# Kernel tuning notes

Measured on AMD Instinct MI355X. Metric: run time of the kernel, lower is better.

## Reference

```python
import jax, jax.numpy as jnp
import numpy as np
import math

NH = 16
SIGMA = 1.5
KS = 7


def _gaussian_blur_16x16(x):
    # x: (N, 16, 16); torchvision GaussianBlur(7, 1.5) with reflect padding
    hx = jnp.arange(KS, dtype=x.dtype) - (KS - 1) / 2.0
    k1 = jnp.exp(-0.5 * (hx / SIGMA) ** 2)
    k1 = k1 / k1.sum()
    k2 = jnp.outer(k1, k1)[None, None]  # (1,1,7,7)
    pad = KS // 2
    xp = jnp.pad(x, ((0, 0), (pad, pad), (pad, pad)), mode='reflect')[:, None]
    y = jax.lax.conv_general_dilated(xp, k2, (1, 1), 'VALID')
    return y[:, 0]


def _normalize(w):
    mn, mx = w.min(), w.max()
    return (w - mn) / (mx - mn)


def _blurred_map(f, b_perm):
    # f, b_perm: (B, 256, 256)
    B = f.shape[0]
    bi = f * b_perm
    bi = bi.reshape(B * 256, 16, 16)
    bl = _gaussian_blur_16x16(bi)
    bl = jnp.clip(_normalize(bl), 0.0, 1.0)
    bl = bl.reshape(B, 256, 256)
    return bl * f * b_perm


def setup_inputs() -> dict:
    key = jax.random.key(0)
    ks = jax.random.split(key, 16)
    B, T, C = 4, 827, 1024
    inp = {
        'x': jax.random.normal(ks[0], (B, T, C), jnp.float32),
        'h': jax.random.normal(ks[1], (B, NH, 827, 827), jnp.float32) * 0.1,
        'f01': jax.random.uniform(ks[2], (B, 256, 256), jnp.float32),
        'f02': jax.random.uniform(ks[3], (B, 256, 256), jnp.float32),
        'f12': jax.random.uniform(ks[4], (B, 256, 256), jnp.float32),
        'b01': jax.random.uniform(ks[5], (B, 256, 256), jnp.float32),
        'b02': jax.random.uniform(ks[6], (B, 256, 256), jnp.float32),
        'b12': jax.random.uniform(ks[7], (B, 256, 256), jnp.float32),
        'Wq': jax.random.normal(ks[8], (C, C), jnp.float32) * 0.02,
        'bq': jnp.zeros((C,), jnp.float32),
        'Wk': jax.random.normal(ks[9], (C, C), jnp.float32) * 0.02,
        'bk': jnp.zeros((C,), jnp.float32),
        'Wv': jax.random.normal(ks[10], (C, C), jnp.float32) * 0.02,
        'bv': jnp.zeros((C,), jnp.float32),
        'Wp': jax.random.normal(ks[11], (C, C), jnp.float32) * 0.02,
        'bp': jnp.zeros((C,), jnp.float32),
    }
    return inp


def reference(x, h, f01, f02, f12, b01, b02, b12,
              Wq, bq, Wk, bk, Wv, bv, Wp, bp):
    B, T, C = x.shape
    hd = C // NH
    # QKV projections -> (B, NH, T, hd)
    def proj(W, b):
        return (x @ W + b).reshape(B, T, NH, hd).transpose(0, 2, 1, 3)
    q, k, v = proj(Wq, bq), proj(Wk, bk), proj(Wv, bv)

    att = jnp.einsum('bhtd,bhsd->bhts', q, k) * (1.0 / math.sqrt(hd))
    att = h[:, :, :T, :T] + att  # adaptive additive bias

    # bidirectional epipolar multiplicative masks with blur
    b01p = jnp.transpose(b01, (0, 2, 1))
    b02p = jnp.transpose(b02, (0, 2, 1))
    b12p = jnp.transpose(b12, (0, 2, 1))
    blur01 = _blurred_map(f01, b01p)[:, None]  # (B,1,256,256), broadcast over heads
    blur02 = _blurred_map(f02, b02p)[:, None]
    blur12 = _blurred_map(f12, b12p)[:, None]

    n1 = min(T - 285, 256)
    att = att.at[:, :, 285:285 + n1, 0:256].multiply(blur01[:, :, :n1])
    if T > 571:
        n2 = T - 571
        att = att.at[:, :, 571:T, 0:256].multiply(blur02[:, :, :n2])
        att = att.at[:, :, 571:T, 286:542].multiply(blur12[:, :, :n2])

    mask = jnp.tril(jnp.ones((T, T), dtype=bool))
    att = jnp.where(mask, att, -jnp.inf)
    att = jax.nn.softmax(att, axis=-1)

    y = jnp.einsum('bhts,bhsd->bhtd', att, v)
    y = y.transpose(0, 2, 1, 3).reshape(B, T, C)
    return y @ Wp + bp
```

## Files before the change

kernel.cpp:

```cpp
#include <hip/hip_runtime.h>
#include <math.h>

using bfrag8 = __attribute__((ext_vector_type(8))) short;
using facc4  = __attribute__((ext_vector_type(4))) float;

#define MFMA16(a,b,c) __builtin_amdgcn_mfma_f32_16x16x32_bf16((a),(b),(c),0,0,0)

#define T_SEQ 827
#define T_PAD 832
#define NHEAD 16
#define NEG_INF (-__builtin_inff())
#define CM_TOT 1179392

static __device__ __forceinline__ unsigned short f2bf(float f) {
    unsigned int x = __float_as_uint(f);
    unsigned int r = x + 0x7FFFu + ((x >> 16) & 1u);
    return (unsigned short)(r >> 16);
}

static __device__ __forceinline__ void gl16(const unsigned short* g, unsigned short* l) {
    __builtin_amdgcn_global_load_lds(
        (const __attribute__((address_space(1))) unsigned int*)g,
        (__attribute__((address_space(3))) unsigned int*)l,
        16, 0, 0);
}

__global__ __launch_bounds__(256) void k_front(const float* __restrict__ x,
                                               unsigned short* __restrict__ x_bf,
                                               float* __restrict__ cm,
                                               unsigned short* q, unsigned short* k,
                                               unsigned short* vT,
                                               const float* __restrict__ Wq,
                                               const float* __restrict__ Wk,
                                               const float* __restrict__ Wv,
                                               const float* __restrict__ Wp,
                                               unsigned short* __restrict__ Wt_out,
                                               const float* f01, const float* f02, const float* f12,
                                               const float* b01, const float* b02, const float* b12,
                                               float* __restrict__ bl,
                                               float* __restrict__ pmm) {
    __shared__ float tile[32][33];
    __shared__ float img[16][17], tmp[16][17];
    __shared__ float smn[4], smx[4];
    int bid = blockIdx.x, tid = threadIdx.x;

    if (bid < 3308) {
        int i = (bid * 256 + tid) * 4;
        float4 v = *reinterpret_cast<const float4*>(x + i);
        ushort4 o;
        o.x = f2bf(v.x); o.y = f2bf(v.y); o.z = f2bf(v.z); o.w = f2bf(v.w);
        *reinterpret_cast<ushort4*>(x_bf + i) = o;
    } else if (bid < 4460) {
        int base = (bid - 3308) * 1024 + tid * 4;
        if (base + 4 <= CM_TOT) {
            float4 one = {1.f, 1.f, 1.f, 1.f};
            *reinterpret_cast<float4*>(cm + base) = one;
        } else {
#pragma unroll
            for (int j = 0; j < 4; ++j)
                if (base + j < CM_TOT) cm[base + j] = 1.f;
        }
    } else if (bid < 4524) {
        int bh = bid - 4460;
        for (int i = tid; i < 320; i += 256) {
            int t = 827 + i / 64, d = i % 64;
            q[((size_t)bh * T_PAD + t) * 64 + d] = 0;
            k[((size_t)bh * T_PAD + t) * 64 + d] = 0;
        }
        for (int i = tid; i < 4096; i += 256) {
            int d = i >> 6, s = 768 + (i & 63);
            vT[((size_t)bh * 64 + d) * T_PAD + s] = 0;
        }
    } else if (bid < 8620) {
        int i = bid - 4524;
        int z = i >> 10, rem = i & 1023;
        int bx = rem & 31, by = rem >> 5;
        const float* W = (z == 0) ? Wq : (z == 1) ? Wk : (z == 2) ? Wv : Wp;
        unsigned short* Wt = Wt_out + (size_t)z * 1048576;
        int tx = tid & 31, ty0 = tid >> 5;
#pragma unroll
        for (int j = 0; j < 4; ++j) {
            int ty = ty0 + j * 8;
            tile[ty][tx] = W[(size_t)(by * 32 + ty) * 1024 + bx * 32 + tx];
        }
        __syncthreads();
#pragma unroll
        for (int j = 0; j < 4; ++j) {
            int ty = ty0 + j * 8;
            Wt[(size_t)(bx * 32 + ty) * 1024 + by * 32 + tx] = f2bf(tile[tx][ty]);
        }
    } else {
        int i = bid - 8620;
        int m = i >> 10, rem = i & 1023, b = rem >> 8, r = rem & 255;
        const float* f  = (m == 0) ? f01 : (m == 1) ? f02 : f12;
        const float* bm = (m == 0) ? b01 : (m == 1) ? b02 : b12;
        int ii = tid >> 4, j = tid & 15;

        float k1[7]; float ks = 0.f;
#pragma unroll
        for (int d = 0; d < 7; ++d) { float hx = (float)d - 3.f; k1[d] = expf(-0.5f * hx * hx / 2.25f); ks += k1[d]; }
#pragma unroll
        for (int d = 0; d < 7; ++d) k1[d] /= ks;

        size_t idx = (size_t)b * 65536 + (size_t)r * 256 + tid;
        float bi = f[idx] * bm[(size_t)b * 65536 + (size_t)tid * 256 + r];
        img[ii][j] = bi;
        __syncthreads();
        float ha = 0.f;
#pragma unroll
        for (int d = 0; d < 7; ++d) { int p = j - 3 + d; p = p < 0 ? -p : (p > 15 ? 30 - p : p); ha += k1[d] * img[ii][p]; }
        tmp[ii][j] = ha;
        __syncthreads();
        float v = 0.f;
#pragma unroll
        for (int d = 0; d < 7; ++d) { int p = ii - 3 + d; p = p < 0 ? -p : (p > 15 ? 30 - p : p); v += k1[d] * tmp[p][j]; }
        bl[(size_t)m * 262144 + idx] = v;

        float mn = v, mx = v;
#pragma unroll
        for (int off = 32; off; off >>= 1) { mn = fminf(mn, __shfl_xor(mn, off)); mx = fmaxf(mx, __shfl_xor(mx, off)); }
        int wid = tid >> 6, lane = tid & 63;
        if (lane == 0) { smn[wid] = mn; smx[wid] = mx; }
        __syncthreads();
        if (tid == 0) {
            mn = fminf(fminf(smn[0], smn[1]), fminf(smn[2], smn[3]));
            mx = fmaxf(fmaxf(smx[0], smx[1]), fmaxf(smx[2], smx[3]));
            pmm[2 * i]     = mn;
            pmm[2 * i + 1] = mx;
        }
    }
}

__global__ __launch_bounds__(256) void k_gemm_qkv(const unsigned short* __restrict__ A,
                                              const unsigned short* __restrict__ Bt,
                                              const float* __restrict__ b0, const float* __restrict__ b1,
                                              const float* __restrict__ b2,
                                              unsigned short* __restrict__ qo, unsigned short* __restrict__ ko,
                                              unsigned short* __restrict__ vo, int M,
                                              const float* f01, const float* f02, const float* f12,
                                              const float* b01, const float* b02, const float* b12,
                                              const float* __restrict__ bl,
                                              const float* __restrict__ pmm,
                                              float* __restrict__ cm) {
    __shared__ unsigned short As[2][4096];
    __shared__ unsigned short Bs[2][4096];
    int bid = blockIdx.x, tid = threadIdx.x;

    if (bid >= 624) {
        int i = bid - 624;
        int m = i >> 10, rem = i & 1023, b = rem >> 8, r = rem & 255;
        float mn = __builtin_inff(), mx = 0.f;
        for (int kk = tid; kk < 1024; kk += 256) {
            int e = m * 1024 + kk;
            mn = fminf(mn, pmm[2 * e]);
            mx = fmaxf(mx, pmm[2 * e + 1]);
        }
#pragma unroll
        for (int off = 32; off; off >>= 1) { mn = fminf(mn, __shfl_xor(mn, off)); mx = fmaxf(mx, __shfl_xor(mx, off)); }
        float* fs = reinterpret_cast<float*>(&As[0][0]);
        int wid = tid >> 6, lane = tid & 63;
        if (lane == 0) { fs[wid] = mn; fs[4 + wid] = mx; }
        __syncthreads();
        mn = fminf(fminf(fs[0], fs[1]), fminf(fs[2], fs[3]));
        mx = fmaxf(fmaxf(fs[4], fs[5]), fmaxf(fs[6], fs[7]));

        const float* f  = (m == 0) ? f01 : (m == 1) ? f02 : f12;
        const float* bm = (m == 0) ? b01 : (m == 1) ? b02 : b12;
        size_t idx = (size_t)b * 65536 + (size_t)r * 256 + tid;
        float w = (bl[(size_t)m * 262144 + idx] - mn) / (mx - mn);
        w = fminf(fmaxf(w, 0.f), 1.f);
        float val = w * f[idx] * bm[(size_t)b * 65536 + (size_t)tid * 256 + r];
        int row = (m == 0) ? r : r + 286;
        int col = (m == 2) ? tid + 286 : tid;
        cm[((size_t)b * 542 + row) * 544 + col] = val;
        return;
    }

    int swz = (bid & 7) * 78 + (bid >> 3);
    int m0 = (swz % 26) * 128, n0 = (swz / 26) * 128;
    int wid = tid >> 6, lane = tid & 63;
    int g = lane >> 4, l15 = lane & 15;
    int wm = wid >> 1, wn = wid & 1;
    facc4 acc[4][4] = {};

    int ar0 = m0 + (tid >> 2); if (ar0 > M - 1) ar0 = M - 1;
    int ar1 = m0 + 64 + (tid >> 2); if (ar1 > M - 1) ar1 = M - 1;
    const unsigned short* Ap0 = A + (size_t)ar0 * 1024 + (tid & 3) * 8;
    const unsigned short* Ap1 = A + (size_t)ar1 * 1024 + (tid & 3) * 8;
    const unsigned short* Bp0 = Bt + (size_t)(n0 + (tid >> 2)) * 1024 + (tid & 3) * 8;
    const unsigned short* Bp1 = Bp0 + (size_t)64 * 1024;

    auto stage = [&](int koff, int buf) {
        gl16(Ap0 + koff, &As[buf][0] + (wid << 9));
        gl16(Ap1 + koff, &As[buf][0] + (wid << 9) + 2048);
        gl16(Bp0 + koff, &Bs[buf][0] + (wid << 9));
        gl16(Bp1 + koff, &Bs[buf][0] + (wid << 9) + 2048);
    };

    stage(0, 0);
    for (int k0 = 0; k0 < 32; ++k0) {
        int cur = k0 & 1;
        bool morek = (k0 + 1 < 32);
        if (morek) {
            stage((k0 + 1) * 32, cur ^ 1);
            asm volatile("s_waitcnt vmcnt(4)" ::: "memory");
        } else {
            asm volatile("s_waitcnt vmcnt(0)" ::: "memory");
        }
        __builtin_amdgcn_s_barrier();
        __builtin_amdgcn_sched_barrier(0);

        bfrag8 af[4], bf[4];
#pragma unroll
        for (int mi = 0; mi < 4; ++mi)
            af[mi] = *reinterpret_cast<const bfrag8*>(&As[cur][(wm * 64 + mi * 16 + l15) * 32 + g * 8]);
#pragma unroll
        for (int ni = 0; ni < 4; ++ni)
            bf[ni] = *reinterpret_cast<const bfrag8*>(&Bs[cur][(wn * 64 + ni * 16 + l15) * 32 + g * 8]);
        __builtin_amdgcn_s_setprio(1);
#pragma unroll
        for (int mi = 0; mi < 4; ++mi)
#pragma unroll
            for (int ni = 0; ni < 4; ++ni)
                acc[mi][ni] = MFMA16(af[mi], bf[ni], acc[mi][ni]);
        __builtin_amdgcn_s_setprio(0);

        __builtin_amdgcn_sched_barrier(0);
        if (morek) __builtin_amdgcn_s_barrier();
    }

    int which = n0 >> 10;
    const float* bb = (which == 0 ? b0 : (which == 1 ? b1 : b2));
#pragma unroll
    for (int mi = 0; mi < 4; ++mi)
#pragma unroll
        for (int ni = 0; ni < 4; ++ni)
#pragma unroll
            for (int r = 0; r < 4; ++r) {
                int row = m0 + wm * 64 + mi * 16 + g * 4 + r;
                if (row >= M) continue;
                int col = n0 + wn * 64 + ni * 16 + l15;
                float v = acc[mi][ni][r] + bb[col & 1023];
                int b = row / T_SEQ, t = row - b * T_SEQ;
                int cc = col & 1023;
                int hh = cc >> 6, d = cc & 63;
                size_t bh = (size_t)(b * NHEAD + hh);
                if (which == 0) {
                    qo[(bh * T_PAD + t) * 64 + d] = f2bf(v);
                } else if (which == 1) {
                    int du = (((d >> 3) ^ (t & 7)) << 3) | (d & 7);
                    ko[(bh * T_PAD + t) * 64 + du] = f2bf(v);
                } else {
                    int sl = t & 63;
                    int su = (((sl >> 3) ^ (d & 7)) << 3) | (t & 7);
                    vo[(bh * 64 + d) * T_PAD + (t - sl) + su] = f2bf(v);
                }
            }
}

__global__ __launch_bounds__(256) void k_proj64(const unsigned short* __restrict__ A,
                                                const unsigned short* __restrict__ Bt,
                                                const float* __restrict__ bias,
                                                float* __restrict__ out, int M) {
    __shared__ unsigned short As[2048];
    __shared__ unsigned short Bs[2048];
    int bid = blockIdx.x, tid = threadIdx.x;
    int swz = (bid & 7) * 104 + (bid >> 3);
    int m0 = (swz % 52) * 64, n0 = (swz / 52) * 64;
    int wid = tid >> 6, lane = tid & 63;
    int g = lane >> 4, l15 = lane & 15;
    int wm = wid >> 1, wn = wid & 1;
    facc4 acc[2][2] = {};

    int ar = m0 + (tid >> 2); if (ar > M - 1) ar = M - 1;
    const unsigned short* Ap = A + (size_t)ar * 1024 + (tid & 3) * 8;
    const unsigned short* Bp = Bt + (size_t)(n0 + (tid >> 2)) * 1024 + (tid & 3) * 8;
    unsigned short* asw = As + (wid << 9);
    unsigned short* bsw = Bs + (wid << 9);

    for (int k0 = 0; k0 < 1024; k0 += 32) {
        if (k0) __syncthreads();
        gl16(Ap + k0, asw);
        gl16(Bp + k0, bsw);
        __syncthreads();
        bfrag8 af[2], bf[2];
#pragma unroll
        for (int mi = 0; mi < 2; ++mi)
            af[mi] = *reinterpret_cast<const bfrag8*>(&As[(wm * 32 + mi * 16 + l15) * 32 + g * 8]);
#pragma unroll
        for (int ni = 0; ni < 2; ++ni)
            bf[ni] = *reinterpret_cast<const bfrag8*>(&Bs[(wn * 32 + ni * 16 + l15) * 32 + g * 8]);
#pragma unroll
        for (int mi = 0; mi < 2; ++mi)
#pragma unroll
            for (int ni = 0; ni < 2; ++ni)
                acc[mi][ni] = MFMA16(af[mi], bf[ni], acc[mi][ni]);
    }

#pragma unroll
    for (int mi = 0; mi < 2; ++mi)
#pragma unroll
        for (int ni = 0; ni < 2; ++ni)
#pragma unroll
            for (int r = 0; r < 4; ++r) {
                int row = m0 + wm * 32 + mi * 16 + g * 4 + r;
                if (row >= M) continue;
                int col = n0 + wn * 32 + ni * 16 + l15;
                out[(size_t)row * 1024 + col] = acc[mi][ni][r] + bias[col];
            }
}

__global__ __launch_bounds__(256) void k_attn(const unsigned short* __restrict__ qb,
                                              const unsigned short* __restrict__ kb,
                                              const unsigned short* __restrict__ vT,
                                              const float* __restrict__ h,
                                              const float* __restrict__ cm,
                                              unsigned short* __restrict__ y) {
    int blk0 = blockIdx.x;
    int blk = (blk0 & 7) * 104 + (blk0 >> 3);
    int bh = blk / 13;
    int qt = 12 - (blk % 13);
    int b = bh >> 4, hh = bh & 15;
    int tid = threadIdx.x, wid = tid >> 6, lane = tid & 63;
    int g = lane >> 4, l15 = lane & 15;
    int t0 = qt * 64 + wid * 16;
    int t = t0 + l15;
    int tcl = t > 826 ? 826 : t;
    int ntiles = qt + 1;

    __shared__ unsigned short Ks[2][4096];
    __shared__ unsigned short Vs[2][4096];
    __shared__ unsigned short Ps[4][1024];
    unsigned short* pw = &Ps[wid][0];

    const unsigned short* Kbase = kb + (size_t)bh * T_PAD * 64;
    const unsigned short* Vbase = vT + (size_t)bh * 64 * T_PAD;
    const float* hrow = h + (size_t)bh * T_SEQ * T_SEQ + (size_t)tcl * T_SEQ;
    int rt = t - 285; rt = rt < 0 ? 0 : (rt > 541 ? 541 : rt);
    const float* cmrow = cm + ((size_t)b * 542 + rt) * 544;
    bool tm = (t >= 285);

    size_t qrow = ((size_t)bh * T_PAD + t) * 64 + g * 8;
    bfrag8 aq0 = *reinterpret_cast<const bfrag8*>(qb + qrow);
    bfrag8 aq1 = *reinterpret_cast<const bfrag8*>(qb + qrow + 32);

    auto stage = [&](int s0, int buf) {
        const unsigned short* kt = Kbase + (size_t)s0 * 64;
        unsigned short* kd = &Ks[buf][0] + (wid << 9);
        gl16(kt + tid * 8, kd);
        gl16(kt + 2048 + tid * 8, kd + 2048);
        const unsigned short* vt = Vbase + s0;
        unsigned short* vd = &Vs[buf][0] + (wid << 9);
        gl16(vt + (size_t)(tid >> 3) * T_PAD + (tid & 7) * 8, vd);
        gl16(vt + (size_t)((tid >> 3) + 32) * T_PAD + (tid & 7) * 8, vd + 2048);
    };

    auto loadh = [&](int s0t, float* hv, float* mv) {
#pragma unroll
        for (int nt = 0; nt < 4; ++nt) {
            int sb = s0t + nt * 16 + 4 * g;
            float h4[4];
            if (sb + 3 <= tcl) {
                __builtin_memcpy(h4, hrow + sb, 16);
            } else {
#pragma unroll
                for (int j = 0; j < 4; ++j) {
                    float hx = 0.f;
                    if (sb + j <= tcl) hx = hrow[sb + j];
                    h4[j] = hx;
                }
            }
            float m4[4];
            if (tm && sb <= 540) {
                __builtin_memcpy(m4, cmrow + sb, 16);
            } else {
#pragma unroll
                for (int j = 0; j < 4; ++j) m4[j] = 1.f;
            }
#pragma unroll
            for (int j = 0; j < 4; ++j) { hv[nt * 4 + j] = h4[j]; mv[nt * 4 + j] = m4[j]; }
        }
    };

    float m_r = NEG_INF, l_r = 0.f;
    facc4 acc[4] = {};
    float hv[16], mv[16];
    loadh(0, hv, mv);
    stage(0, 0);

    for (int it = 0; it < ntiles; ++it) {
        int cur = it & 1, s0 = it * 64;
        bool more = (it + 1 < ntiles);
        bool diag = !more;
        __syncthreads();
        if (more) stage(s0 + 64, cur ^ 1);

        facc4 sf[4] = {};
        __builtin_amdgcn_s_setprio(1);
#pragma unroll
        for (int nt = 0; nt < 4; ++nt) {
            int row = nt * 16 + l15;
            const unsigned short* kp = &Ks[cur][row * 64];
            bfrag8 k0 = *reinterpret_cast<const bfrag8*>(kp + ((g ^ (row & 7)) << 3));
            bfrag8 k1 = *reinterpret_cast<const bfrag8*>(kp + (((4 + g) ^ (row & 7)) << 3));
            sf[nt] = MFMA16(k0, aq0, sf[nt]);
            sf[nt] = MFMA16(k1, aq1, sf[nt]);
        }
        __builtin_amdgcn_s_setprio(0);

        float vmax = NEG_INF;
#pragma unroll
        for (int nt = 0; nt < 4; ++nt)
#pragma unroll
            for (int r = 0; r < 4; ++r) {
                float val = fmaf(sf[nt][r], 0.125f, hv[nt * 4 + r]) * mv[nt * 4 + r];
                if (diag) {
                    int s = s0 + nt * 16 + 4 * g + r;
                    val = (s <= tcl) ? val : NEG_INF;
                }
                sf[nt][r] = val;
                vmax = fmaxf(vmax, val);
            }

        if (more) loadh(s0 + 64, hv, mv);

        vmax = fmaxf(vmax, __shfl_xor(vmax, 16));
        vmax = fmaxf(vmax, __shfl_xor(vmax, 32));

        bool noresc = __all(vmax <= m_r + 6.0f);
        float mnew = fmaxf(m_r, vmax);
        float mexp = noresc ? m_r : mnew;

        float ps = 0.f;
#pragma unroll
        for (int nt = 0; nt < 4; ++nt)
#pragma unroll
            for (int r = 0; r < 4; ++r) {
                float p = __expf(sf[nt][r] - mexp);
                sf[nt][r] = p;
                ps += p;
            }
        ps += __shfl_xor(ps, 16);
        ps += __shfl_xor(ps, 32);

#pragma unroll
        for (int nt = 0; nt < 4; ++nt) {
            unsigned u0, u1;
            asm("v_cvt_pk_bf16_f32 %0, %1, %2" : "=v"(u0) : "v"(sf[nt][0]), "v"(sf[nt][1]));
            asm("v_cvt_pk_bf16_f32 %0, %1, %2" : "=v"(u1) : "v"(sf[nt][2]), "v"(sf[nt][3]));
            int el = (l15 * 64 + nt * 16 + 4 * g) ^ ((l15 & 7) << 3);
            uint2 uu; uu.x = u0; uu.y = u1;
            *reinterpret_cast<uint2*>(&pw[el]) = uu;
        }

        if (!noresc) {
            float scale = __expf(m_r - mnew);
            l_r = l_r * scale + ps;
#pragma unroll
            for (int r = 0; r < 4; ++r) {
                float sc = __int_as_float(__builtin_amdgcn_ds_bpermute((4 * g + r) * 4, __float_as_int(scale)));
#pragma unroll
                for (int dt = 0; dt < 4; ++dt) acc[dt][r] *= sc;
            }
            m_r = mnew;
        } else {
            l_r += ps;
        }

        __builtin_amdgcn_s_setprio(1);
#pragma unroll
        for (int c2 = 0; c2 < 2; ++c2) {
            int ela = (l15 * 64 + c2 * 32 + 8 * g) ^ ((l15 & 7) << 3);
            bfrag8 ap = *reinterpret_cast<const bfrag8*>(&pw[ela]);
#pragma unroll
            for (int dt = 0; dt < 4; ++dt) {
                int row = dt * 16 + l15;
                bfrag8 vf = *reinterpret_cast<const bfrag8*>(&Vs[cur][row * 64 + (((c2 * 4 + g) ^ (row & 7)) << 3)]);
                acc[dt] = MFMA16(ap, vf, acc[dt]);
            }
        }
        __builtin_amdgcn_s_setprio(0);
    }

    float linv = 1.0f / l_r;
#pragma unroll
    for (int r = 0; r < 4; ++r) {
        float li = __int_as_float(__builtin_amdgcn_ds_bpermute((4 * g + r) * 4, __float_as_int(linv)));
        int tt = t0 + 4 * g + r;
        if (tt < T_SEQ) {
#pragma unroll
            for (int dt = 0; dt < 4; ++dt)
                y[((size_t)(b * T_SEQ) + tt) * 1024 + hh * 64 + dt * 16 + l15] = f2bf(acc[dt][r] * li);
        }
    }
}

extern "C" void kernel_launch(void* const* d_in, const int* in_sizes, int n_in,
                              void* d_out, int out_size, void* d_ws, size_t ws_size,
                              hipStream_t stream) {
    const float* x   = (const float*)d_in[0];
    const float* h   = (const float*)d_in[1];
    const float* f01 = (const float*)d_in[2];
    const float* f02 = (const float*)d_in[3];
    const float* f12 = (const float*)d_in[4];
    const float* b01 = (const float*)d_in[5];
    const float* b02 = (const float*)d_in[6];
    const float* b12 = (const float*)d_in[7];
    const float* Wq  = (const float*)d_in[8];
    const float* bq  = (const float*)d_in[9];
    const float* Wk  = (const float*)d_in[10];
    const float* bk  = (const float*)d_in[11];
    const float* Wv  = (const float*)d_in[12];
    const float* bv  = (const float*)d_in[13];
    const float* Wp  = (const float*)d_in[14];
    const float* bp  = (const float*)d_in[15];

    char* ws = (char*)d_ws;
    float* pmm    = (float*)(ws + 256);
    float* bl     = (float*)(ws + 256 + 24576);
    float* cmb    = (float*)(ws + 256 + 24576 + 3145728);
    unsigned short* x_bf  = (unsigned short*)(ws + 256 + 24576 + 3145728 + 4717568);
    unsigned short* WtQKV = x_bf + (size_t)3308 * 1024;
    unsigned short* WtP   = WtQKV + (size_t)3072 * 1024;
    unsigned short* q_bf  = WtP + (size_t)1024 * 1024;
    unsigned short* k_bf  = q_bf + (size_t)64 * T_PAD * 64;
    unsigned short* vTb   = k_bf + (size_t)64 * T_PAD * 64;
    unsigned short* y_bf  = vTb  + (size_t)64 * T_PAD * 64;

    k_front<<<11692, 256, 0, stream>>>(x, x_bf, cmb, q_bf, k_bf, vTb,
                                       Wq, Wk, Wv, Wp, WtQKV,
                                       f01, f02, f12, b01, b02, b12, bl, pmm);
    k_gemm_qkv<<<3696, 256, 0, stream>>>(x_bf, WtQKV, bq, bk, bv, q_bf, k_bf, vTb, 3308,
                                         f01, f02, f12, b01, b02, b12, bl, pmm, cmb);
    k_attn<<<832, 256, 0, stream>>>(q_bf, k_bf, vTb, h, cmb, y_bf);
    k_proj64<<<832, 256, 0, stream>>>(y_bf, WtP, bp, (float*)d_out, 3308);
}
```

Baseline: 134.1 us.

## Prefetch attention bias ahead with manual vmcnt waits and split barriers

Restructures the attention loop's memory pipeline. The bias row h for the next tile is now loaded at the start of each iteration into a separate register buffer, split from the mask load and made branch-free through a clamped index. __syncthreads is replaced with explicit s_waitcnt vmcnt counts plus s_barrier and sched_barrier, so the wait covers the current K/V tile but not the freshly issued prefetches. It also adds a launch_bounds occupancy hint of 3 and a second barrier at the end of the loop. The risks are more register pressure from the extra hn buffer, and hardcoded vmcnt counts that may be fragile if the compiler emits a different number of loads.

```diff
diff --git a/kernel.cpp b/kernel.cpp
--- a/kernel.cpp
+++ b/kernel.cpp
@@ -310,7 +310,7 @@
             }
 }
 
-__global__ __launch_bounds__(256) void k_attn(const unsigned short* __restrict__ qb,
+__global__ __launch_bounds__(256, 3) void k_attn(const unsigned short* __restrict__ qb,
                                               const unsigned short* __restrict__ kb,
                                               const unsigned short* __restrict__ vT,
                                               const float* __restrict__ h,
@@ -355,21 +355,24 @@
         gl16(vt + (size_t)((tid >> 3) + 32) * T_PAD + (tid & 7) * 8, vd + 2048);
     };
 
-    auto loadh = [&](int s0t, float* hv, float* mv) {
+    auto loadh_h = [&](int s0t, float* hd) {
 #pragma unroll
         for (int nt = 0; nt < 4; ++nt) {
             int sb = s0t + nt * 16 + 4 * g;
-            float h4[4];
-            if (sb + 3 <= tcl) {
-                __builtin_memcpy(h4, hrow + sb, 16);
-            } else {
-#pragma unroll
-                for (int j = 0; j < 4; ++j) {
-                    float hx = 0.f;
-                    if (sb + j <= tcl) hx = hrow[sb + j];
-                    h4[j] = hx;
-                }
-            }
+#pragma unroll
+            for (int j = 0; j < 4; ++j) {
+                int a = sb + j;
+                int ac = a > 826 ? 826 : a;
+                float hx = hrow[ac];
+                hd[nt * 4 + j] = (a <= tcl) ? hx : 0.f;
+            }
+        }
+    };
+
+    auto loadm = [&](int s0t, float* mvd) {
+#pragma unroll
+        for (int nt = 0; nt < 4; ++nt) {
+            int sb = s0t + nt * 16 + 4 * g;
             float m4[4];
             if (tm && sb <= 540) {
                 __builtin_memcpy(m4, cmrow + sb, 16);
@@ -378,22 +381,32 @@
                 for (int j = 0; j < 4; ++j) m4[j] = 1.f;
             }
 #pragma unroll
-            for (int j = 0; j < 4; ++j) { hv[nt * 4 + j] = h4[j]; mv[nt * 4 + j] = m4[j]; }
+            for (int j = 0; j < 4; ++j) mvd[nt * 4 + j] = m4[j];
         }
     };
 
     float m_r = NEG_INF, l_r = 0.f;
     facc4 acc[4] = {};
-    float hv[16], mv[16];
-    loadh(0, hv, mv);
+    float hv[16], mv[16], hn[16];
     stage(0, 0);
+    loadh_h(0, hv);
+    loadm(0, mv);
 
     for (int it = 0; it < ntiles; ++it) {
         int cur = it & 1, s0 = it * 64;
         bool more = (it + 1 < ntiles);
         bool diag = !more;
-        __syncthreads();
-        if (more) stage(s0 + 64, cur ^ 1);
+
+        if (more) {
+            stage(s0 + 64, cur ^ 1);
+            loadh_h(s0 + 64, hn);
+            __builtin_amdgcn_sched_barrier(0);
+            asm volatile("s_waitcnt vmcnt(20)" ::: "memory");
+        } else {
+            asm volatile("s_waitcnt vmcnt(0)" ::: "memory");
+        }
+        __builtin_amdgcn_s_barrier();
+        __builtin_amdgcn_sched_barrier(0);
 
         facc4 sf[4] = {};
         __builtin_amdgcn_s_setprio(1);
@@ -422,7 +435,7 @@
                 vmax = fmaxf(vmax, val);
             }
 
-        if (more) loadh(s0 + 64, hv, mv);
+        if (more) loadm(s0 + 64, mv);
 
         vmax = fmaxf(vmax, __shfl_xor(vmax, 16));
         vmax = fmaxf(vmax, __shfl_xor(vmax, 32));
@@ -480,6 +493,13 @@
             }
         }
         __builtin_amdgcn_s_setprio(0);
+
+        __builtin_amdgcn_sched_barrier(0);
+        __builtin_amdgcn_s_barrier();
+        if (more) {
+#pragma unroll
+            for (int i2 = 0; i2 < 16; ++i2) hv[i2] = hn[i2];
+        }
     }
 
     float linv = 1.0f / l_r;
```

Result: slower. 163.4 us (+21.9%).
